# Performance work log

Measured on AMD Instinct MI355X. Metric: run time of the kernel, lower is better.

Reference implementation:

```python
import jax, jax.numpy as jnp
import numpy as np

RCUT = 6.0      # cutoff radius
AXIS = 16       # axis_neuron
NORM = 64.0     # normalizer = avg_neighbors + 1 (precomputed stat)
EPS = 1e-15
NTYPES = 2


def _embed(h, W0, b0, W1, b1, W2, b2):
    # tiny per-type-pair embedding MLP: scalar sr -> C channels
    h = jnp.tanh(h @ W0 + b0)
    h = jnp.tanh(h @ W1 + b1)
    return jnp.tanh(h @ W2 + b2)


def _forward(coord_3N, box_33, srmean, srstd, xrsrstd, Gbias, Ebias,
             emb_W0, emb_b0, emb_W1, emb_b1, emb_W2, emb_b2,
             fit_W0, fit_b0, fit_W1, fit_b1, fit_W2, fit_b2, n1):
    N = coord_3N.shape[1]
    L = jnp.diagonal(box_33)  # orthorhombic box lengths (3,)
    # relative coords with minimum-image convention: x[d,i,j] = c[d,j] - c[d,i]
    x_3NM = coord_3N[:, None, :] - coord_3N[:, :, None]
    x_3NM = x_3NM - L[:, None, None] * jnp.round(x_3NM / L[:, None, None])
    eye = jnp.eye(N, dtype=bool)
    r_NM = jnp.sqrt(jnp.where(eye, 1.0, (x_3NM ** 2).sum(0)))  # diag masked for safe grad
    # smooth switching / r  (DeepPot-SE style sr)
    u = r_NM / RCUT
    sw = jnp.where((r_NM < RCUT) & (~eye), ((-6.0 * u + 15.0) * u - 10.0) * u ** 3 + 1.0, 0.0)
    sr_NM = sw / r_NM
    rsr_NM = sr_NM / r_NM
    idx = (0, n1, N)  # contiguous type boundaries (atoms sorted by type)
    rows_sr, rows_rsr, rows_emb = [], [], []
    for i in range(NTYPES):
        sr_i = sr_NM[idx[i]:idx[i + 1]]
        rows_sr.append(sr_i / srstd[i])
        rows_rsr.append(rsr_NM[idx[i]:idx[i + 1]] / xrsrstd[i])
        srn_i = (sr_i - srmean[i]) / srstd[i]
        blocks = []
        for j in range(NTYPES):
            p = NTYPES * i + j  # type-pair index
            blocks.append(_embed(srn_i[:, idx[j]:idx[j + 1], None],
                                 emb_W0[p], emb_b0[p], emb_W1[p], emb_b1[p], emb_W2[p], emb_b2[p]))
        rows_emb.append(jnp.concatenate(blocks, axis=1))
    srbias_NM = jnp.concatenate(rows_sr, axis=0)
    R_3NM = (jnp.concatenate(rows_rsr, axis=0)[None] + EPS) * x_3NM  # e3norm = 1
    embed_NMC = jnp.concatenate(rows_emb, axis=0)
    # weighted reductions over neighbor axis M (einsum avoids the 3*N*M*C temp)
    Ginv_NC = jnp.einsum('nm,nmc->nc', srbias_NM, embed_NMC) / NORM
    Geqv_3NC = jnp.einsum('dnm,nmc->dnc', R_3NM, embed_NMC) / NORM
    G_4NC = jnp.concatenate([(Ginv_NC + Gbias)[None], Geqv_3NC], axis=0)
    # equivariant outer-product descriptor: Feat[n,a,c] = sum_k G[k,n,c]*G[k,n,a]
    Feat_NX = jnp.einsum('knc,kna->nac', G_4NC, G_4NC[:, :, :AXIS]).reshape(N, -1)
    energy = jnp.zeros((), dtype=Feat_NX.dtype)
    for i in range(NTYPES):
        h = Feat_NX[idx[i]:idx[i + 1]]
        h = jnp.tanh(h @ fit_W0[i] + fit_b0[i])
        h = jnp.tanh(h @ fit_W1[i] + fit_b1[i])
        h = h @ fit_W2[i] + fit_b2[i]
        energy = energy + (h + Ebias[i]).sum()
    return energy


def setup_inputs() -> dict:
    key = jax.random.key(0)
    ks = jax.random.split(key, 20)
    N, N1, BOXL = 1024, 512, 20.0
    W = (16, 32, 64)
    X, F = AXIS * W[-1], 128

    def wt(k, shape, fan_in):
        return jax.random.normal(k, shape, jnp.float32) / np.float32(np.sqrt(fan_in))

    return {
        'coord_3N': jax.random.uniform(ks[0], (3, N), jnp.float32) * BOXL,
        'box_33': BOXL * jnp.eye(3, dtype=jnp.float32),
        'srmean': 0.1 * jax.random.uniform(ks[1], (NTYPES,), jnp.float32),
        'srstd': 0.5 + jax.random.uniform(ks[2], (NTYPES,), jnp.float32),
        'xrsrstd': 0.5 + jax.random.uniform(ks[3], (NTYPES,), jnp.float32),
        'Gbias': 0.1 * jax.random.normal(ks[4], (W[2],), jnp.float32),
        'Ebias': jax.random.normal(ks[5], (NTYPES,), jnp.float32),
        'emb_W0': wt(ks[6], (4, 1, W[0]), 1),
        'emb_b0': 0.1 * jax.random.normal(ks[7], (4, W[0]), jnp.float32),
        'emb_W1': wt(ks[8], (4, W[0], W[1]), W[0]),
        'emb_b1': 0.1 * jax.random.normal(ks[9], (4, W[1]), jnp.float32),
        'emb_W2': wt(ks[10], (4, W[1], W[2]), W[1]),
        'emb_b2': 0.1 * jax.random.normal(ks[11], (4, W[2]), jnp.float32),
        'fit_W0': wt(ks[12], (NTYPES, X, F), X),
        'fit_b0': 0.1 * jax.random.normal(ks[13], (NTYPES, F), jnp.float32),
        'fit_W1': wt(ks[14], (NTYPES, F, F), F),
        'fit_b1': 0.1 * jax.random.normal(ks[15], (NTYPES, F), jnp.float32),
        'fit_W2': wt(ks[16], (NTYPES, F, 1), F),
        'fit_b2': 0.1 * jax.random.normal(ks[17], (NTYPES, 1), jnp.float32),
        'n1': N1,
    }


def reference(coord_3N, box_33, srmean, srstd, xrsrstd, Gbias, Ebias,
              emb_W0, emb_b0, emb_W1, emb_b1, emb_W2, emb_b2,
              fit_W0, fit_b0, fit_W1, fit_b1, fit_W2, fit_b2, n1):
    return _forward(coord_3N, box_33, srmean, srstd, xrsrstd, Gbias, Ebias,
                    emb_W0, emb_b0, emb_W1, emb_b1, emb_W2, emb_b2,
                    fit_W0, fit_b0, fit_W1, fit_b1, fit_W2, fit_b2, n1)
```

## Files before the change

### kernel.cpp

```cpp
#include <hip/hip_runtime.h>

#define RCUT 6.0f

typedef _Float16 h2 __attribute__((ext_vector_type(2)));
typedef _Float16 h8 __attribute__((ext_vector_type(8)));
typedef float    f4 __attribute__((ext_vector_type(4)));

__device__ __forceinline__ float fast_tanh(float x) {
    float e = __expf(2.0f * x);
    return 1.0f - 2.0f * __builtin_amdgcn_rcpf(e + 1.0f);
}

__device__ __forceinline__ h2 pkh(float a, float b) {
#if __has_builtin(__builtin_amdgcn_cvt_pkrtz)
    union { __fp16 __attribute__((ext_vector_type(2))) r; h2 h; } u;
    u.r = __builtin_amdgcn_cvt_pkrtz(a, b);
    return u.h;
#else
    h2 r; r.x = (_Float16)a; r.y = (_Float16)b; return r;
#endif
}

__global__ __launch_bounds__(256, 4) void k_embed(
    const float* __restrict__ coord, const float* __restrict__ box,
    const float* __restrict__ srmean, const float* __restrict__ srstd,
    const float* __restrict__ xrsrstd, const float* __restrict__ Gbias,
    const float* __restrict__ eW0, const float* __restrict__ eb0,
    const float* __restrict__ eW1, const float* __restrict__ eb1,
    const float* __restrict__ eW2, const float* __restrict__ eb2,
    const int* __restrict__ n1p,
    const float* __restrict__ fW0, const float* __restrict__ fW1,
    h2* __restrict__ feat, _Float16* __restrict__ W0ht,
    _Float16* __restrict__ W1ht, unsigned int* __restrict__ counter, int N)
{
    const int nb  = blockIdx.x;
    const int tid = threadIdx.x;

    __shared__ struct { float w0[2][16], b0[2][16]; } sw;
    __shared__ _Float16 s_h0[128][24];
    __shared__ _Float16 s_h1[128][40];
    __shared__ __align__(16) _Float16 s_ef[4][4][64][8];
    __shared__ float s_coef[4][128];
    __shared__ unsigned short s_nbr[512];
    __shared__ float s_g4[256];
    __shared__ int   s_wcnt[4], s_wcnt0[4];

    if (nb >= N) {
        const int b = nb - N;
        if (b == 0 && tid == 0) *counter = 0u;
        float (*s_t)[33] = reinterpret_cast<float(*)[33]>(&s_ef[0][0][0][0]);
        if (b < 256) {
            int type = b >> 7, tb = b & 127;
            int ki = tb >> 2, ci = tb & 3;
            const float* src = fW0 + (size_t)type * 131072;
            int c = tid & 31, r0 = (tid >> 5) * 4;
            #pragma unroll
            for (int q = 0; q < 4; q++)
                s_t[r0 + q][c] = src[(size_t)(ki * 32 + r0 + q) * 128 + ci * 32 + c];
            __syncthreads();
            _Float16* dst = W0ht + (size_t)type * 131072;
            int kk = tid & 31, c0 = (tid >> 5) * 4;
            #pragma unroll
            for (int q = 0; q < 4; q++)
                dst[(size_t)(ci * 32 + c0 + q) * 1024 + ki * 32 + kk] = (_Float16)s_t[kk][c0 + q];
        } else {
            int b2v = b - 256;
            int type = b2v >> 4, tb = b2v & 15;
            int ki = tb >> 2, ci = tb & 3;
            const float* src = fW1 + (size_t)type * 16384;
            int c = tid & 31, r0 = (tid >> 5) * 4;
            #pragma unroll
            for (int q = 0; q < 4; q++)
                s_t[r0 + q][c] = src[(size_t)(ki * 32 + r0 + q) * 128 + ci * 32 + c];
            __syncthreads();
            _Float16* dst = W1ht + (size_t)type * 16384;
            int kk = tid & 31, c0 = (tid >> 5) * 4;
            #pragma unroll
            for (int q = 0; q < 4; q++)
                dst[(size_t)(ci * 32 + c0 + q) * 128 + ki * 32 + kk] = (_Float16)s_t[kk][c0 + q];
        }
        return;
    }

    const int n  = nb;
    const int n1 = *n1p;
    const int ti = (n >= n1) ? 1 : 0;

    for (int t = tid; t < 32; t += 256) { int j = t >> 4, f = t & 15;
        sw.w0[j][f] = eW0[(2 * ti + j) * 16 + f];
        sw.b0[j][f] = eb0[(2 * ti + j) * 16 + f]; }

    const int wid = tid >> 6, lane = tid & 63;
    const int l15 = lane & 15, lk = lane >> 4;

    h8 bf[2][4];
    float b2r[2][4];
    #pragma unroll
    for (int j = 0; j < 2; j++) {
        const float* w2g = eW2 + (size_t)(2 * ti + j) * 2048;
        #pragma unroll
        for (int nt = 0; nt < 4; nt++) {
            h8 v;
            #pragma unroll
            for (int r = 0; r < 8; r++)
                v[r] = (_Float16)w2g[(8 * lk + r) * 64 + nt * 16 + l15];
            bf[j][nt] = v;
            b2r[j][nt] = eb2[(2 * ti + j) * 64 + nt * 16 + l15];
        }
    }
    h8 w1f[2][2];
    float b1r[2][2];
    #pragma unroll
    for (int j = 0; j < 2; j++) {
        const float* w1g = eW1 + (size_t)(2 * ti + j) * 512;
        #pragma unroll
        for (int nt1 = 0; nt1 < 2; nt1++) {
            h8 v = {};
            if (lk < 2) {
                #pragma unroll
                for (int r = 0; r < 8; r++)
                    v[r] = (_Float16)w1g[(8 * lk + r) * 32 + 16 * nt1 + l15];
            }
            w1f[j][nt1] = v;
            b1r[j][nt1] = eb1[(2 * ti + j) * 32 + 16 * nt1 + l15];
        }
    }

    const float Lx = box[0], Ly = box[4], Lz = box[8];
    const float iLx = 1.0f / Lx, iLy = 1.0f / Ly, iLz = 1.0f / Lz;
    const float xn = coord[n], yn = coord[N + n], zn = coord[2 * N + n];

    {
        unsigned long long bal[4];
        int wtotal = 0, wtotal0 = 0;
        const int mystart = wid * 256;
        #pragma unroll
        for (int r = 0; r < 4; r++) {
            int m = mystart + r * 64 + lane;
            float dx = coord[m] - xn;         dx -= Lx * rintf(dx * iLx);
            float dy = coord[N + m] - yn;     dy -= Ly * rintf(dy * iLy);
            float dz = coord[2 * N + m] - zn; dz -= Lz * rintf(dz * iLz);
            float r2 = dx * dx + dy * dy + dz * dz;
            bool pred = (r2 < RCUT * RCUT) && (m != n);
            bal[r] = __ballot(pred);
            unsigned long long bal0 = __ballot(pred && (m < n1));
            wtotal  += (int)__popcll(bal[r]);
            wtotal0 += (int)__popcll(bal0);
        }
        if (lane == 0) { s_wcnt[wid] = wtotal; s_wcnt0[wid] = wtotal0; }
        __syncthreads();
        int base = 0;
        for (int w = 0; w < wid; w++) base += s_wcnt[w];
        #pragma unroll
        for (int r = 0; r < 4; r++) {
            bool pred = (bal[r] >> lane) & 1ull;
            int pos = (int)__popcll(bal[r] & ((1ull << lane) - 1ull));
            if (pred && (base + pos) < 512)
                s_nbr[base + pos] = (unsigned short)(wid * 256 + r * 64 + lane);
            base += (int)__popcll(bal[r]);
        }
    }
    __syncthreads();
    int cnt  = s_wcnt[0] + s_wcnt[1] + s_wcnt[2] + s_wcnt[3];
    int cnt0 = s_wcnt0[0] + s_wcnt0[1] + s_wcnt0[2] + s_wcnt0[3];
    if (cnt > 512) cnt = 512;

    const float srm  = srmean[ti];
    const float isrs = 1.0f / srstd[ti];
    const float ixrs = 1.0f / xrsrstd[ti];

    const int p  = tid & 127;
    const int hh = tid >> 7;
    const int dummy = (n + 1 < N) ? (n + 1) : 0;

    f4 gacc = {0.0f, 0.0f, 0.0f, 0.0f};
    const f4 zf4 = {0.0f, 0.0f, 0.0f, 0.0f};

    const int ntiles = (cnt + 127) >> 7;
    for (int t = 0; t < ntiles; t++) {
        const int t128 = t << 7;
        __syncthreads();
        {
            const int pi = t128 + p;
            const bool valid = pi < cnt;
            int m = valid ? (int)s_nbr[pi] : dummy;
            float dx = coord[m] - xn;         dx -= Lx * rintf(dx * iLx);
            float dy = coord[N + m] - yn;     dy -= Ly * rintf(dy * iLy);
            float dz = coord[2 * N + m] - zn; dz -= Lz * rintf(dz * iLz);
            float r2 = dx * dx + dy * dy + dz * dz;
            float r  = sqrtf(r2);
            float rinv = __builtin_amdgcn_rcpf(r);
            float u  = r * (1.0f / RCUT);
            float u3 = u * u * u;
            float sw_ = ((-6.0f * u + 15.0f) * u - 10.0f) * u3 + 1.0f;
            if (!valid) sw_ = 0.0f;
            float sr  = sw_ * rinv;
            float srn = (sr - srm) * isrs;
            if (hh == 0) {
                float csr = valid ? sr * isrs : 0.0f;
                float crs = valid ? (sr * rinv * ixrs + 1e-15f) : 0.0f;
                s_coef[0][p] = csr;
                s_coef[1][p] = crs * dx;
                s_coef[2][p] = crs * dy;
                s_coef[3][p] = crs * dz;
            }
            const int j = (m >= n1) ? 1 : 0;
            h8 v;
            #pragma unroll
            for (int q = 0; q < 8; q++) {
                int f = 8 * hh + q;
                v[q] = (_Float16)fast_tanh(fmaf(srn, sw.w0[j][f], sw.b0[j][f]));
            }
            *(h8*)&s_h0[p][8 * hh] = v;
        }
        __syncthreads();

        {
            #pragma unroll
            for (int mt2 = 0; mt2 < 2; mt2++) {
                const int mt  = 2 * wid + mt2;
                const int row = 16 * mt + l15;
                h8 a = {};
                if (lk < 2) a = *(const h8*)&s_h0[row][8 * lk];
                const int gpb = 16 * mt;
                const bool need0 = (t128 + gpb) < cnt0;
                const bool need1 = (t128 + gpb + 15) >= cnt0;
                #pragma unroll
                for (int nt1 = 0; nt1 < 2; nt1++) {
                    f4 d0 = zf4, d1 = zf4;
                    if (need0) d0 = __builtin_amdgcn_mfma_f32_16x16x32_f16(a, w1f[0][nt1], zf4, 0, 0, 0);
                    if (need1) d1 = __builtin_amdgcn_mfma_f32_16x16x32_f16(a, w1f[1][nt1], zf4, 0, 0, 0);
                    #pragma unroll
                    for (int r = 0; r < 4; r++) {
                        int gp = gpb + 4 * lk + r;
                        bool is0 = (t128 + gp) < cnt0;
                        float dv = is0 ? d0[r] : d1[r];
                        float hv = fast_tanh(dv + (is0 ? b1r[0][nt1] : b1r[1][nt1]));
                        s_h1[gp][16 * nt1 + l15] = (_Float16)hv;
                    }
                }
            }
        }
        __syncthreads();

        {
            #pragma unroll
            for (int mt2 = 0; mt2 < 2; mt2++) {
                const int mt  = 2 * wid + mt2;
                const int row = 16 * mt + l15;
                h8 a = *(const h8*)&s_h1[row][8 * lk];
                const int gpb = 16 * mt;
                const bool need0 = (t128 + gpb) < cnt0;
                const bool need1 = (t128 + gpb + 15) >= cnt0;
                #pragma unroll
                for (int nt = 0; nt < 4; nt++) {
                    f4 d0 = zf4, d1 = zf4;
                    if (need0) d0 = __builtin_amdgcn_mfma_f32_16x16x32_f16(a, bf[0][nt], zf4, 0, 0, 0);
                    if (need1) d1 = __builtin_amdgcn_mfma_f32_16x16x32_f16(a, bf[1][nt], zf4, 0, 0, 0);
                    #pragma unroll
                    for (int r = 0; r < 4; r++) {
                        int gp = gpb + 4 * lk + r;
                        bool is0 = (t128 + gp) < cnt0;
                        float dv = is0 ? d0[r] : d1[r];
                        float ev = fast_tanh(dv + (is0 ? b2r[0][nt] : b2r[1][nt]));
                        s_ef[nt][gp >> 5][l15 + 16 * ((gp & 31) >> 3)][gp & 7] = (_Float16)ev;
                    }
                }
            }
        }
        __syncthreads();

        {
            #pragma unroll
            for (int ks = 0; ks < 4; ks++) {
                h8 ac;
                #pragma unroll
                for (int r = 0; r < 8; r++) {
                    int kk = 32 * ks + 8 * lk + r;
                    float cv = (l15 < 4) ? s_coef[l15][kk] : 0.0f;
                    ac[r] = (_Float16)cv;
                }
                h8 eb = *(const h8*)&s_ef[wid][ks][lane][0];
                gacc = __builtin_amdgcn_mfma_f32_16x16x32_f16(ac, eb, gacc, 0, 0, 0);
            }
        }
    }

    if (lane < 16) {
        #pragma unroll
        for (int r = 0; r < 4; r++) {
            float gv = gacc[r] * (1.0f / 64.0f);
            if (r == 0) gv += Gbias[16 * wid + lane];
            s_g4[r * 64 + 16 * wid + lane] = gv;
        }
    }
    __syncthreads();
    {
        h2* outp = feat + (size_t)n * 512;
        #pragma unroll
        for (int q = 0; q < 2; q++) {
            int o2 = tid + 256 * q;
            int a = o2 >> 5;
            int c = (2 * o2) & 63;
            float ga0 = s_g4[a],       ga1 = s_g4[64 + a];
            float ga2 = s_g4[128 + a], ga3 = s_g4[192 + a];
            float s0 = ga0 * s_g4[c];
            s0 = fmaf(ga1, s_g4[64 + c],  s0);
            s0 = fmaf(ga2, s_g4[128 + c], s0);
            s0 = fmaf(ga3, s_g4[192 + c], s0);
            float s1 = ga0 * s_g4[c + 1];
            s1 = fmaf(ga1, s_g4[64 + c + 1],  s1);
            s1 = fmaf(ga2, s_g4[128 + c + 1], s1);
            s1 = fmaf(ga3, s_g4[192 + c + 1], s1);
            outp[o2] = pkh(s0, s1);
        }
    }
}

__global__ __launch_bounds__(512) void k_fit(
    const _Float16* __restrict__ featf, const _Float16* __restrict__ W0ht,
    const _Float16* __restrict__ W1ht,
    const float* __restrict__ b0, const float* __restrict__ b1,
    const float* __restrict__ W2, const float* __restrict__ b2,
    const float* __restrict__ Ebias, const int* __restrict__ n1p,
    unsigned int* __restrict__ counter, float* __restrict__ slots,
    float* __restrict__ out)
{
    __shared__ _Float16 s_A[64 * 128];
    __shared__ _Float16 s_B[128 * 128];
    __shared__ _Float16 s_h[64 * 128];
    __shared__ float s_part[8];

    const int tid  = threadIdx.x;
    const int lane = tid & 63, w = tid >> 6;
    const int mt = w >> 1, nh = w & 1;
    const int l15 = lane & 15, lk = lane >> 4;
    const int n0 = blockIdx.x * 64;
    const int n1 = *n1p;
    const int ia = (n0 >= n1) ? 1 : 0;

    const _Float16* W0t = W0ht + (size_t)ia * 131072;
    const _Float16* W1t = W1ht + (size_t)ia * 16384;

    f4 acc[4];
    #pragma unroll
    for (int nt = 0; nt < 4; nt++) acc[nt] = (f4)0.0f;

    for (int kt = 0; kt < 8; kt++) {
        __syncthreads();
        {
            int r = tid >> 3, ub = (tid & 7) * 2;
            const h8* g = (const h8*)(featf + (size_t)(n0 + r) * 1024 + kt * 128);
            #pragma unroll
            for (int q = 0; q < 2; q++) {
                int u = ub + q;
                *(h8*)&s_A[r * 128 + ((u ^ (r & 15)) << 3)] = g[u];
            }
        }
        {
            int c = tid >> 2, ub = (tid & 3) * 4;
            const h8* g = (const h8*)(W0t + (size_t)c * 1024 + kt * 128);
            #pragma unroll
            for (int q = 0; q < 4; q++) {
                int u = ub + q;
                *(h8*)&s_B[c * 128 + ((u ^ (c & 15)) << 3)] = g[u];
            }
        }
        __syncthreads();
        #pragma unroll
        for (int ks = 0; ks < 4; ks++) {
            const int row = mt * 16 + l15;
            h8 a = *(const h8*)&s_A[row * 128 + (((ks * 4 + lk) ^ (row & 15)) << 3)];
            #pragma unroll
            for (int nt = 0; nt < 4; nt++) {
                const int c = nh * 64 + nt * 16 + l15;
                h8 bfr = *(const h8*)&s_B[c * 128 + (((ks * 4 + lk) ^ (c & 15)) << 3)];
                acc[nt] = __builtin_amdgcn_mfma_f32_16x16x32_f16(a, bfr, acc[nt], 0, 0, 0);
            }
        }
    }

    #pragma unroll
    for (int nt = 0; nt < 4; nt++) {
        const int c = nh * 64 + nt * 16 + l15;
        const float bias = b0[ia * 128 + c];
        #pragma unroll
        for (int r = 0; r < 4; r++) {
            const int row = mt * 16 + lk * 4 + r;
            float v = fast_tanh(acc[nt][r] + bias);
            s_h[row * 128 + (((c >> 3) ^ (row & 15)) << 3) + (c & 7)] = (_Float16)v;
        }
    }
    __syncthreads();
    {
        int c = tid >> 2, ub = (tid & 3) * 4;
        const h8* g = (const h8*)(W1t + (size_t)c * 128);
        #pragma unroll
        for (int q = 0; q < 4; q++) {
            int u = ub + q;
            *(h8*)&s_B[c * 128 + ((u ^ (c & 15)) << 3)] = g[u];
        }
    }
    __syncthreads();

    f4 acc1[4];
    #pragma unroll
    for (int nt = 0; nt < 4; nt++) acc1[nt] = (f4)0.0f;
    #pragma unroll
    for (int ks = 0; ks < 4; ks++) {
        const int row = mt * 16 + l15;
        h8 a = *(const h8*)&s_h[row * 128 + (((ks * 4 + lk) ^ (row & 15)) << 3)];
        #pragma unroll
        for (int nt = 0; nt < 4; nt++) {
            const int c = nh * 64 + nt * 16 + l15;
            h8 bfr = *(const h8*)&s_B[c * 128 + (((ks * 4 + lk) ^ (c & 15)) << 3)];
            acc1[nt] = __builtin_amdgcn_mfma_f32_16x16x32_f16(a, bfr, acc1[nt], 0, 0, 0);
        }
    }

    float p = 0.0f;
    #pragma unroll
    for (int nt = 0; nt < 4; nt++) {
        const int c = nh * 64 + nt * 16 + l15;
        const float bias = b1[ia * 128 + c];
        const float w2v  = W2[ia * 128 + c];
        #pragma unroll
        for (int r = 0; r < 4; r++)
            p += fast_tanh(acc1[nt][r] + bias) * w2v;
    }
    #pragma unroll
    for (int m = 1; m < 64; m <<= 1) p += __shfl_xor(p, m);
    if (lane == 0) s_part[w] = p;
    __syncthreads();
    if (tid == 0) {
        float e = ((s_part[0] + s_part[1]) + (s_part[2] + s_part[3]))
                + ((s_part[4] + s_part[5]) + (s_part[6] + s_part[7]))
                + 64.0f * (b2[ia] + Ebias[ia]);
        slots[blockIdx.x] = e;
        __threadfence();
        unsigned int old = atomicAdd(counter, 1u);
        if (old == 15u) {
            __threadfence();
            float tot = 0.0f;
            #pragma unroll
            for (int i = 0; i < 16; i++)
                tot += __hip_atomic_load(&slots[i], __ATOMIC_RELAXED, __HIP_MEMORY_SCOPE_AGENT);
            out[0] = tot;
        }
    }
}

extern "C" void kernel_launch(void* const* d_in, const int* in_sizes, int n_in,
                              void* d_out, int out_size, void* d_ws, size_t ws_size,
                              hipStream_t stream) {
    const float* coord   = (const float*)d_in[0];
    const float* box     = (const float*)d_in[1];
    const float* srmean  = (const float*)d_in[2];
    const float* srstd   = (const float*)d_in[3];
    const float* xrsrstd = (const float*)d_in[4];
    const float* Gbias   = (const float*)d_in[5];
    const float* Ebias   = (const float*)d_in[6];
    const float* eW0     = (const float*)d_in[7];
    const float* eb0     = (const float*)d_in[8];
    const float* eW1     = (const float*)d_in[9];
    const float* eb1     = (const float*)d_in[10];
    const float* eW2     = (const float*)d_in[11];
    const float* eb2     = (const float*)d_in[12];
    const float* fW0     = (const float*)d_in[13];
    const float* fb0     = (const float*)d_in[14];
    const float* fW1     = (const float*)d_in[15];
    const float* fb1     = (const float*)d_in[16];
    const float* fW2     = (const float*)d_in[17];
    const float* fb2     = (const float*)d_in[18];
    const int*   n1p     = (const int*)d_in[19];

    const int N = in_sizes[0] / 3;
    h2*       featbuf = (h2*)d_ws;
    _Float16* W0ht = (_Float16*)((char*)d_ws + (size_t)2 * 1024 * 1024);
    _Float16* W1ht = W0ht + 2 * 131072;
    char* tail = (char*)d_ws + (size_t)(2 * 1024 + 512 + 64) * 1024;
    unsigned int* counter = (unsigned int*)tail;
    float*        slots   = (float*)(tail + 64);

    k_embed<<<N + 288, 256, 0, stream>>>(coord, box, srmean, srstd, xrsrstd, Gbias,
                                         eW0, eb0, eW1, eb1, eW2, eb2, n1p,
                                         fW0, fW1, featbuf, W0ht, W1ht, counter, N);
    k_fit<<<N / 64, 512, 0, stream>>>((const _Float16*)featbuf, W0ht, W1ht,
                                      fb0, fb1, fW2, fb2, Ebias, n1p,
                                      counter, slots, (float*)d_out);
}
```

Baseline: 41.04 us.

## Process two atoms per embed block and split-K the fitting GEMM

The embed kernel now handles two centre atoms per block and shares the neighbour scan across both. It precomputes per-neighbour coefficients into shared memory once, so each tile no longer recomputes them from coordinates. Embedding weights are staged in shared memory instead of registers, and occupancy drops to three blocks per SM. The fit kernel switches to 16-row tiles with split-K across waves, reads operands straight from global memory and reduces through shared memory, which puts more blocks on the grid at the cost of extra reduction traffic.

```diff
diff --git a/kernel.cpp b/kernel.cpp
--- a/kernel.cpp
+++ b/kernel.cpp
@@ -2,26 +2,26 @@
 
 #define RCUT 6.0f
 
-typedef _Float16 h2 __attribute__((ext_vector_type(2)));
-typedef _Float16 h8 __attribute__((ext_vector_type(8)));
-typedef float    f4 __attribute__((ext_vector_type(4)));
+typedef _Float16 h2v __attribute__((ext_vector_type(2)));
+typedef _Float16 h8  __attribute__((ext_vector_type(8)));
+typedef float    f4  __attribute__((ext_vector_type(4)));
 
 __device__ __forceinline__ float fast_tanh(float x) {
     float e = __expf(2.0f * x);
     return 1.0f - 2.0f * __builtin_amdgcn_rcpf(e + 1.0f);
 }
 
-__device__ __forceinline__ h2 pkh(float a, float b) {
+__device__ __forceinline__ h2v pkh(float a, float b) {
 #if __has_builtin(__builtin_amdgcn_cvt_pkrtz)
-    union { __fp16 __attribute__((ext_vector_type(2))) r; h2 h; } u;
+    union { __fp16 __attribute__((ext_vector_type(2))) r; h2v h; } u;
     u.r = __builtin_amdgcn_cvt_pkrtz(a, b);
     return u.h;
 #else
-    h2 r; r.x = (_Float16)a; r.y = (_Float16)b; return r;
+    h2v r; r.x = (_Float16)a; r.y = (_Float16)b; return r;
 #endif
 }
 
-__global__ __launch_bounds__(256, 4) void k_embed(
+__global__ __launch_bounds__(256, 3) void k_embed(
     const float* __restrict__ coord, const float* __restrict__ box,
     const float* __restrict__ srmean, const float* __restrict__ srstd,
     const float* __restrict__ xrsrstd, const float* __restrict__ Gbias,
@@ -30,23 +30,26 @@
     const float* __restrict__ eW2, const float* __restrict__ eb2,
     const int* __restrict__ n1p,
     const float* __restrict__ fW0, const float* __restrict__ fW1,
-    h2* __restrict__ feat, _Float16* __restrict__ W0ht,
+    h2v* __restrict__ feat, _Float16* __restrict__ W0ht,
     _Float16* __restrict__ W1ht, unsigned int* __restrict__ counter, int N)
 {
     const int nb  = blockIdx.x;
     const int tid = threadIdx.x;
-
-    __shared__ struct { float w0[2][16], b0[2][16]; } sw;
-    __shared__ _Float16 s_h0[128][24];
-    __shared__ _Float16 s_h1[128][40];
+    const int NB  = N >> 1;
+
+    __shared__ float s_w0[2][16], s_b0[2][16];
+    __shared__ __align__(16) _Float16 s_srn[1024];
+    __shared__ __align__(16) _Float16 s_cf[4][1024];
+    __shared__ __align__(16) _Float16 s_h1[128][32];
     __shared__ __align__(16) _Float16 s_ef[4][4][64][8];
-    __shared__ float s_coef[4][128];
-    __shared__ unsigned short s_nbr[512];
-    __shared__ float s_g4[256];
-    __shared__ int   s_wcnt[4], s_wcnt0[4];
-
-    if (nb >= N) {
-        const int b = nb - N;
+    __shared__ unsigned short s_nbr[1024];
+    __shared__ float s_g4[2][256];
+    __shared__ __align__(16) _Float16 w1t[2][32][24];
+    __shared__ __align__(16) _Float16 w2t[2][64][40];
+    __shared__ int s_wA[4], s_wB[4];
+
+    if (nb >= NB) {
+        const int b = nb - NB;
         if (b == 0 && tid == 0) *counter = 0u;
         float (*s_t)[33] = reinterpret_cast<float(*)[33]>(&s_ef[0][0][0][0]);
         if (b < 256) {
@@ -64,8 +67,7 @@
             for (int q = 0; q < 4; q++)
                 dst[(size_t)(ci * 32 + c0 + q) * 1024 + ki * 32 + kk] = (_Float16)s_t[kk][c0 + q];
         } else {
-            int b2v = b - 256;
-            int type = b2v >> 4, tb = b2v & 15;
+            int b2v = b - 256, type = b2v >> 4, tb = b2v & 15;
             int ki = tb >> 2, ci = tb & 3;
             const float* src = fW1 + (size_t)type * 16384;
             int c = tid & 31, r0 = (tid >> 5) * 4;
@@ -82,242 +84,248 @@
         return;
     }
 
-    const int n  = nb;
+    const int nA = 2 * nb, nBt = 2 * nb + 1;
     const int n1 = *n1p;
-    const int ti = (n >= n1) ? 1 : 0;
-
-    for (int t = tid; t < 32; t += 256) { int j = t >> 4, f = t & 15;
-        sw.w0[j][f] = eW0[(2 * ti + j) * 16 + f];
-        sw.b0[j][f] = eb0[(2 * ti + j) * 16 + f]; }
-
+    const int ti = (nA >= n1) ? 1 : 0;
     const int wid = tid >> 6, lane = tid & 63;
     const int l15 = lane & 15, lk = lane >> 4;
 
-    h8 bf[2][4];
-    float b2r[2][4];
+    for (int t = tid; t < 32; t += 256) { int j = t >> 4, f = t & 15;
+        s_w0[j][f] = eW0[(2 * ti + j) * 16 + f];
+        s_b0[j][f] = eb0[(2 * ti + j) * 16 + f]; }
+    for (int idx = tid; idx < 1024; idx += 256) {
+        int j = idx >> 9, r = idx & 511, f = r >> 5, g = r & 31;
+        w1t[j][g][f] = (_Float16)eW1[(2 * ti + j) * 512 + f * 32 + g];
+    }
+    for (int idx = tid; idx < 4096; idx += 256) {
+        int j = idx >> 11, r = idx & 2047, g = r >> 6, c = r & 63;
+        w2t[j][c][g] = (_Float16)eW2[(2 * ti + j) * 2048 + g * 64 + c];
+    }
+    float b1r[2][2], b2r[2][4];
     #pragma unroll
     for (int j = 0; j < 2; j++) {
-        const float* w2g = eW2 + (size_t)(2 * ti + j) * 2048;
-        #pragma unroll
-        for (int nt = 0; nt < 4; nt++) {
-            h8 v;
-            #pragma unroll
-            for (int r = 0; r < 8; r++)
-                v[r] = (_Float16)w2g[(8 * lk + r) * 64 + nt * 16 + l15];
-            bf[j][nt] = v;
-            b2r[j][nt] = eb2[(2 * ti + j) * 64 + nt * 16 + l15];
-        }
-    }
-    h8 w1f[2][2];
-    float b1r[2][2];
-    #pragma unroll
-    for (int j = 0; j < 2; j++) {
-        const float* w1g = eW1 + (size_t)(2 * ti + j) * 512;
-        #pragma unroll
-        for (int nt1 = 0; nt1 < 2; nt1++) {
-            h8 v = {};
-            if (lk < 2) {
-                #pragma unroll
-                for (int r = 0; r < 8; r++)
-                    v[r] = (_Float16)w1g[(8 * lk + r) * 32 + 16 * nt1 + l15];
-            }
-            w1f[j][nt1] = v;
-            b1r[j][nt1] = eb1[(2 * ti + j) * 32 + 16 * nt1 + l15];
-        }
+        #pragma unroll
+        for (int q = 0; q < 2; q++) b1r[j][q] = eb1[(2 * ti + j) * 32 + 16 * q + l15];
+        #pragma unroll
+        for (int q = 0; q < 4; q++) b2r[j][q] = eb2[(2 * ti + j) * 64 + 16 * q + l15];
     }
 
     const float Lx = box[0], Ly = box[4], Lz = box[8];
     const float iLx = 1.0f / Lx, iLy = 1.0f / Ly, iLz = 1.0f / Lz;
-    const float xn = coord[n], yn = coord[N + n], zn = coord[2 * N + n];
-
-    {
-        unsigned long long bal[4];
-        int wtotal = 0, wtotal0 = 0;
-        const int mystart = wid * 256;
-        #pragma unroll
-        for (int r = 0; r < 4; r++) {
-            int m = mystart + r * 64 + lane;
-            float dx = coord[m] - xn;         dx -= Lx * rintf(dx * iLx);
-            float dy = coord[N + m] - yn;     dy -= Ly * rintf(dy * iLy);
-            float dz = coord[2 * N + m] - zn; dz -= Lz * rintf(dz * iLz);
-            float r2 = dx * dx + dy * dy + dz * dz;
-            bool pred = (r2 < RCUT * RCUT) && (m != n);
-            bal[r] = __ballot(pred);
-            unsigned long long bal0 = __ballot(pred && (m < n1));
-            wtotal  += (int)__popcll(bal[r]);
-            wtotal0 += (int)__popcll(bal0);
-        }
-        if (lane == 0) { s_wcnt[wid] = wtotal; s_wcnt0[wid] = wtotal0; }
-        __syncthreads();
-        int base = 0;
-        for (int w = 0; w < wid; w++) base += s_wcnt[w];
-        #pragma unroll
-        for (int r = 0; r < 4; r++) {
-            bool pred = (bal[r] >> lane) & 1ull;
-            int pos = (int)__popcll(bal[r] & ((1ull << lane) - 1ull));
-            if (pred && (base + pos) < 512)
-                s_nbr[base + pos] = (unsigned short)(wid * 256 + r * 64 + lane);
-            base += (int)__popcll(bal[r]);
-        }
-    }
-    __syncthreads();
-    int cnt  = s_wcnt[0] + s_wcnt[1] + s_wcnt[2] + s_wcnt[3];
-    int cnt0 = s_wcnt0[0] + s_wcnt0[1] + s_wcnt0[2] + s_wcnt0[3];
-    if (cnt > 512) cnt = 512;
-
+    const float xA = coord[nA], yA = coord[N + nA], zA = coord[2 * N + nA];
+    const float xB = coord[nBt], yB = coord[N + nBt], zB = coord[2 * N + nBt];
     const float srm  = srmean[ti];
     const float isrs = 1.0f / srstd[ti];
     const float ixrs = 1.0f / xrsrstd[ti];
 
-    const int p  = tid & 127;
-    const int hh = tid >> 7;
-    const int dummy = (n + 1 < N) ? (n + 1) : 0;
+    unsigned long long balA[4], balB[4];
+    float dxA[4], dyA[4], dzA[4], r2A[4];
+    float dxB[4], dyB[4], dzB[4], r2B[4];
+    {
+        int wA = 0, wB = 0;
+        const int mystart = wid * 256;
+        #pragma unroll
+        for (int r = 0; r < 4; r++) {
+            int m = mystart + r * 64 + lane;
+            float x = coord[m], y = coord[N + m], z = coord[2 * N + m];
+            float ax = x - xA; ax -= Lx * rintf(ax * iLx);
+            float ay = y - yA; ay -= Ly * rintf(ay * iLy);
+            float az = z - zA; az -= Lz * rintf(az * iLz);
+            float ra = ax * ax + ay * ay + az * az;
+            float bx = x - xB; bx -= Lx * rintf(bx * iLx);
+            float by = y - yB; by -= Ly * rintf(by * iLy);
+            float bz = z - zB; bz -= Lz * rintf(bz * iLz);
+            float rb = bx * bx + by * by + bz * bz;
+            dxA[r] = ax; dyA[r] = ay; dzA[r] = az; r2A[r] = ra;
+            dxB[r] = bx; dyB[r] = by; dzB[r] = bz; r2B[r] = rb;
+            bool pA = (ra < RCUT * RCUT) && (m != nA);
+            bool pB = (rb < RCUT * RCUT) && (m != nBt);
+            balA[r] = __ballot(pA);
+            balB[r] = __ballot(pB);
+            wA += (int)__popcll(balA[r]);
+            wB += (int)__popcll(balB[r]);
+        }
+        if (lane == 0) { s_wA[wid] = wA; s_wB[wid] = wB; }
+    }
+    __syncthreads();
+    int cntA = s_wA[0] + s_wA[1] + s_wA[2] + s_wA[3];
+    int cntB = s_wB[0] + s_wB[1] + s_wB[2] + s_wB[3];
+    int cnt  = cntA + cntB;
+    if (cnt > 1024) cnt = 1024;
+    if (cntA > 1024) cntA = 1024;
+    {
+        int baseA = 0, baseB = cntA;
+        for (int w = 0; w < wid; w++) { baseA += s_wA[w]; baseB += s_wB[w]; }
+        const unsigned long long lt = (1ull << lane) - 1ull;
+        const int mystart = wid * 256;
+        #pragma unroll
+        for (int r = 0; r < 4; r++) {
+            int m = mystart + r * 64 + lane;
+            #pragma unroll
+            for (int cc = 0; cc < 2; cc++) {
+                unsigned long long bal = cc ? balB[r] : balA[r];
+                int base = cc ? baseB : baseA;
+                if ((bal >> lane) & 1ull) {
+                    int pos = base + (int)__popcll(bal & lt);
+                    if (pos < 1024) {
+                        float dx = cc ? dxB[r] : dxA[r];
+                        float dy = cc ? dyB[r] : dyA[r];
+                        float dz = cc ? dzB[r] : dzA[r];
+                        float r2 = cc ? r2B[r] : r2A[r];
+                        float rr = sqrtf(r2);
+                        float rinv = __builtin_amdgcn_rcpf(rr);
+                        float u  = rr * (1.0f / RCUT);
+                        float u3 = u * u * u;
+                        float sw_ = ((-6.0f * u + 15.0f) * u - 10.0f) * u3 + 1.0f;
+                        float sr  = sw_ * rinv;
+                        float crs = sr * rinv * ixrs + 1e-15f;
+                        s_srn[pos]   = (_Float16)((sr - srm) * isrs);
+                        s_cf[0][pos] = (_Float16)(sr * isrs);
+                        s_cf[1][pos] = (_Float16)(crs * dx);
+                        s_cf[2][pos] = (_Float16)(crs * dy);
+                        s_cf[3][pos] = (_Float16)(crs * dz);
+                        s_nbr[pos]   = (unsigned short)m;
+                    }
+                }
+                if (cc) baseB += (int)__popcll(bal);
+                else    baseA += (int)__popcll(bal);
+            }
+        }
+    }
+    __syncthreads();
+    const int ntiles = (cnt + 127) >> 7;
+    for (int i = cnt + tid; i < ntiles * 128; i += 256) {
+        s_srn[i] = (_Float16)0.0f; s_nbr[i] = 0;
+        s_cf[0][i] = (_Float16)0.0f; s_cf[1][i] = (_Float16)0.0f;
+        s_cf[2][i] = (_Float16)0.0f; s_cf[3][i] = (_Float16)0.0f;
+    }
+    __syncthreads();
 
     f4 gacc = {0.0f, 0.0f, 0.0f, 0.0f};
     const f4 zf4 = {0.0f, 0.0f, 0.0f, 0.0f};
 
-    const int ntiles = (cnt + 127) >> 7;
     for (int t = 0; t < ntiles; t++) {
         const int t128 = t << 7;
         __syncthreads();
-        {
-            const int pi = t128 + p;
-            const bool valid = pi < cnt;
-            int m = valid ? (int)s_nbr[pi] : dummy;
-            float dx = coord[m] - xn;         dx -= Lx * rintf(dx * iLx);
-            float dy = coord[N + m] - yn;     dy -= Ly * rintf(dy * iLy);
-            float dz = coord[2 * N + m] - zn; dz -= Lz * rintf(dz * iLz);
-            float r2 = dx * dx + dy * dy + dz * dz;
-            float r  = sqrtf(r2);
-            float rinv = __builtin_amdgcn_rcpf(r);
-            float u  = r * (1.0f / RCUT);
-            float u3 = u * u * u;
-            float sw_ = ((-6.0f * u + 15.0f) * u - 10.0f) * u3 + 1.0f;
-            if (!valid) sw_ = 0.0f;
-            float sr  = sw_ * rinv;
-            float srn = (sr - srm) * isrs;
-            if (hh == 0) {
-                float csr = valid ? sr * isrs : 0.0f;
-                float crs = valid ? (sr * rinv * ixrs + 1e-15f) : 0.0f;
-                s_coef[0][p] = csr;
-                s_coef[1][p] = crs * dx;
-                s_coef[2][p] = crs * dy;
-                s_coef[3][p] = crs * dz;
-            }
-            const int j = (m >= n1) ? 1 : 0;
-            h8 v;
-            #pragma unroll
-            for (int q = 0; q < 8; q++) {
-                int f = 8 * hh + q;
-                v[q] = (_Float16)fast_tanh(fmaf(srn, sw.w0[j][f], sw.b0[j][f]));
-            }
-            *(h8*)&s_h0[p][8 * hh] = v;
+
+        #pragma unroll
+        for (int mt2 = 0; mt2 < 2; mt2++) {
+            const int mt = 2 * wid + mt2;
+            const int row = 16 * mt + l15;
+            const int rp = t128 + row;
+            float srn = (float)s_srn[rp];
+            int jr = (s_nbr[rp] >= n1) ? 1 : 0;
+            h8 a = {};
+            if (lk < 2) {
+                const float* wp = &s_w0[jr][8 * lk];
+                const float* bp = &s_b0[jr][8 * lk];
+                #pragma unroll
+                for (int q = 0; q < 8; q++)
+                    a[q] = (_Float16)fast_tanh(fmaf(srn, wp[q], bp[q]));
+            }
+            #pragma unroll
+            for (int nt1 = 0; nt1 < 2; nt1++) {
+                const int c = 16 * nt1 + l15;
+                h8 b0f = {}, b1f = {};
+                if (lk < 2) {
+                    b0f = *(const h8*)&w1t[0][c][8 * lk];
+                    b1f = *(const h8*)&w1t[1][c][8 * lk];
+                }
+                f4 d0 = __builtin_amdgcn_mfma_f32_16x16x32_f16(a, b0f, zf4, 0, 0, 0);
+                f4 d1 = __builtin_amdgcn_mfma_f32_16x16x32_f16(a, b1f, zf4, 0, 0, 0);
+                #pragma unroll
+                for (int r = 0; r < 4; r++) {
+                    int gp = 16 * mt + 4 * lk + r;
+                    bool is0 = (s_nbr[t128 + gp] < n1);
+                    float hv = fast_tanh((is0 ? d0[r] : d1[r]) + (is0 ? b1r[0][nt1] : b1r[1][nt1]));
+                    int e = 16 * nt1 + l15;
+                    s_h1[gp][(((e >> 3) ^ ((gp >> 1) & 3)) << 3) + (e & 7)] = (_Float16)hv;
+                }
+            }
+        }
+        asm volatile("" ::: "memory");
+        #pragma unroll
+        for (int mt2 = 0; mt2 < 2; mt2++) {
+            const int mt = 2 * wid + mt2;
+            const int row = 16 * mt + l15;
+            h8 a2 = *(const h8*)&s_h1[row][((lk ^ ((row >> 1) & 3)) << 3)];
+            #pragma unroll
+            for (int nt = 0; nt < 4; nt++) {
+                const int c = 16 * nt + l15;
+                h8 w20 = *(const h8*)&w2t[0][c][8 * lk];
+                h8 w21 = *(const h8*)&w2t[1][c][8 * lk];
+                f4 e0 = __builtin_amdgcn_mfma_f32_16x16x32_f16(a2, w20, zf4, 0, 0, 0);
+                f4 e1 = __builtin_amdgcn_mfma_f32_16x16x32_f16(a2, w21, zf4, 0, 0, 0);
+                #pragma unroll
+                for (int r = 0; r < 4; r++) {
+                    int gp = 16 * mt + 4 * lk + r;
+                    bool is0 = (s_nbr[t128 + gp] < n1);
+                    float ev = fast_tanh((is0 ? e0[r] : e1[r]) + (is0 ? b2r[0][nt] : b2r[1][nt]));
+                    s_ef[nt][gp >> 5][l15 + 16 * ((gp & 31) >> 3)][gp & 7] = (_Float16)ev;
+                }
+            }
         }
         __syncthreads();
 
-        {
-            #pragma unroll
-            for (int mt2 = 0; mt2 < 2; mt2++) {
-                const int mt  = 2 * wid + mt2;
-                const int row = 16 * mt + l15;
-                h8 a = {};
-                if (lk < 2) a = *(const h8*)&s_h0[row][8 * lk];
-                const int gpb = 16 * mt;
-                const bool need0 = (t128 + gpb) < cnt0;
-                const bool need1 = (t128 + gpb + 15) >= cnt0;
-                #pragma unroll
-                for (int nt1 = 0; nt1 < 2; nt1++) {
-                    f4 d0 = zf4, d1 = zf4;
-                    if (need0) d0 = __builtin_amdgcn_mfma_f32_16x16x32_f16(a, w1f[0][nt1], zf4, 0, 0, 0);
-                    if (need1) d1 = __builtin_amdgcn_mfma_f32_16x16x32_f16(a, w1f[1][nt1], zf4, 0, 0, 0);
+        #pragma unroll
+        for (int ks = 0; ks < 4; ks++) {
+            const int s = t128 + 32 * ks;
+            h8 ac = {};
+            if (l15 < 8) {
+                const bool rowA = l15 < 4;
+                const int  cr   = rowA ? l15 : (l15 - 4);
+                const bool allA = (s + 31) < cntA;
+                const bool allB = s >= cntA;
+                if ((allA && rowA) || (allB && !rowA)) {
+                    ac = *(const h8*)&s_cf[cr][s + 8 * lk];
+                } else if (!allA && !allB) {
                     #pragma unroll
-                    for (int r = 0; r < 4; r++) {
-                        int gp = gpb + 4 * lk + r;
-                        bool is0 = (t128 + gp) < cnt0;
-                        float dv = is0 ? d0[r] : d1[r];
-                        float hv = fast_tanh(dv + (is0 ? b1r[0][nt1] : b1r[1][nt1]));
-                        s_h1[gp][16 * nt1 + l15] = (_Float16)hv;
+                    for (int r = 0; r < 8; r++) {
+                        int p = s + 8 * lk + r;
+                        bool isA = p < cntA;
+                        if (isA == rowA) ac[r] = s_cf[cr][p];
                     }
                 }
             }
-        }
-        __syncthreads();
-
-        {
-            #pragma unroll
-            for (int mt2 = 0; mt2 < 2; mt2++) {
-                const int mt  = 2 * wid + mt2;
-                const int row = 16 * mt + l15;
-                h8 a = *(const h8*)&s_h1[row][8 * lk];
-                const int gpb = 16 * mt;
-                const bool need0 = (t128 + gpb) < cnt0;
-                const bool need1 = (t128 + gpb + 15) >= cnt0;
-                #pragma unroll
-                for (int nt = 0; nt < 4; nt++) {
-                    f4 d0 = zf4, d1 = zf4;
-                    if (need0) d0 = __builtin_amdgcn_mfma_f32_16x16x32_f16(a, bf[0][nt], zf4, 0, 0, 0);
-                    if (need1) d1 = __builtin_amdgcn_mfma_f32_16x16x32_f16(a, bf[1][nt], zf4, 0, 0, 0);
-                    #pragma unroll
-                    for (int r = 0; r < 4; r++) {
-                        int gp = gpb + 4 * lk + r;
-                        bool is0 = (t128 + gp) < cnt0;
-                        float dv = is0 ? d0[r] : d1[r];
-                        float ev = fast_tanh(dv + (is0 ? b2r[0][nt] : b2r[1][nt]));
-                        s_ef[nt][gp >> 5][l15 + 16 * ((gp & 31) >> 3)][gp & 7] = (_Float16)ev;
-                    }
-                }
-            }
-        }
-        __syncthreads();
-
-        {
-            #pragma unroll
-            for (int ks = 0; ks < 4; ks++) {
-                h8 ac;
-                #pragma unroll
-                for (int r = 0; r < 8; r++) {
-                    int kk = 32 * ks + 8 * lk + r;
-                    float cv = (l15 < 4) ? s_coef[l15][kk] : 0.0f;
-                    ac[r] = (_Float16)cv;
-                }
-                h8 eb = *(const h8*)&s_ef[wid][ks][lane][0];
-                gacc = __builtin_amdgcn_mfma_f32_16x16x32_f16(ac, eb, gacc, 0, 0, 0);
-            }
-        }
-    }
-
-    if (lane < 16) {
+            h8 eb = *(const h8*)&s_ef[wid][ks][lane][0];
+            gacc = __builtin_amdgcn_mfma_f32_16x16x32_f16(ac, eb, gacc, 0, 0, 0);
+        }
+    }
+
+    if (lk < 2) {
+        float* sg = &s_g4[lk][0];
         #pragma unroll
         for (int r = 0; r < 4; r++) {
             float gv = gacc[r] * (1.0f / 64.0f);
-            if (r == 0) gv += Gbias[16 * wid + lane];
-            s_g4[r * 64 + 16 * wid + lane] = gv;
-        }
-    }
-    __syncthreads();
-    {
-        h2* outp = feat + (size_t)n * 512;
+            if (r == 0) gv += Gbias[16 * wid + l15];
+            sg[r * 64 + 16 * wid + l15] = gv;
+        }
+    }
+    __syncthreads();
+    #pragma unroll
+    for (int at = 0; at < 2; at++) {
+        const float* sg = &s_g4[at][0];
+        h2v* outp = feat + (size_t)(2 * nb + at) * 512;
         #pragma unroll
         for (int q = 0; q < 2; q++) {
             int o2 = tid + 256 * q;
-            int a = o2 >> 5;
-            int c = (2 * o2) & 63;
-            float ga0 = s_g4[a],       ga1 = s_g4[64 + a];
-            float ga2 = s_g4[128 + a], ga3 = s_g4[192 + a];
-            float s0 = ga0 * s_g4[c];
-            s0 = fmaf(ga1, s_g4[64 + c],  s0);
-            s0 = fmaf(ga2, s_g4[128 + c], s0);
-            s0 = fmaf(ga3, s_g4[192 + c], s0);
-            float s1 = ga0 * s_g4[c + 1];
-            s1 = fmaf(ga1, s_g4[64 + c + 1],  s1);
-            s1 = fmaf(ga2, s_g4[128 + c + 1], s1);
-            s1 = fmaf(ga3, s_g4[192 + c + 1], s1);
+            int a = o2 >> 5, c = (2 * o2) & 63;
+            float ga0 = sg[a],       ga1 = sg[64 + a];
+            float ga2 = sg[128 + a], ga3 = sg[192 + a];
+            float s0 = ga0 * sg[c];
+            s0 = fmaf(ga1, sg[64 + c],  s0);
+            s0 = fmaf(ga2, sg[128 + c], s0);
+            s0 = fmaf(ga3, sg[192 + c], s0);
+            float s1 = ga0 * sg[c + 1];
+            s1 = fmaf(ga1, sg[64 + c + 1],  s1);
+            s1 = fmaf(ga2, sg[128 + c + 1], s1);
+            s1 = fmaf(ga3, sg[192 + c + 1], s1);
             outp[o2] = pkh(s0, s1);
         }
     }
 }
 
-__global__ __launch_bounds__(512) void k_fit(
+__global__ __launch_bounds__(512, 1) void k_fit(
     const _Float16* __restrict__ featf, const _Float16* __restrict__ W0ht,
     const _Float16* __restrict__ W1ht,
     const float* __restrict__ b0, const float* __restrict__ b1,
@@ -326,126 +334,108 @@
     unsigned int* __restrict__ counter, float* __restrict__ slots,
     float* __restrict__ out)
 {
-    __shared__ _Float16 s_A[64 * 128];
-    __shared__ _Float16 s_B[128 * 128];
-    __shared__ _Float16 s_h[64 * 128];
-    __shared__ float s_part[8];
-
-    const int tid  = threadIdx.x;
+    __shared__ float s_red[4][2][16][64];
+    __shared__ __align__(16) _Float16 s_hd[16][128];
+    __shared__ float s_sum[16][32];
+
+    const int tid = threadIdx.x;
     const int lane = tid & 63, w = tid >> 6;
-    const int mt = w >> 1, nh = w & 1;
+    const int kq = w >> 1, ch = w & 1;
     const int l15 = lane & 15, lk = lane >> 4;
-    const int n0 = blockIdx.x * 64;
-    const int n1 = *n1p;
-    const int ia = (n0 >= n1) ? 1 : 0;
-
-    const _Float16* W0t = W0ht + (size_t)ia * 131072;
-    const _Float16* W1t = W1ht + (size_t)ia * 16384;
-
-    f4 acc[4];
+    const int n0 = blockIdx.x * 16;
+    const int ia = (n0 >= *n1p) ? 1 : 0;
+    const f4 zf4 = {0.0f, 0.0f, 0.0f, 0.0f};
+
+    const _Float16* Ap = featf + (size_t)(n0 + l15) * 1024 + kq * 256;
+    const _Float16* B0 = W0ht + (size_t)ia * 131072 + kq * 256;
+    f4 acc[4] = {zf4, zf4, zf4, zf4};
     #pragma unroll
-    for (int nt = 0; nt < 4; nt++) acc[nt] = (f4)0.0f;
-
-    for (int kt = 0; kt < 8; kt++) {
-        __syncthreads();
-        {
-            int r = tid >> 3, ub = (tid & 7) * 2;
-            const h8* g = (const h8*)(featf + (size_t)(n0 + r) * 1024 + kt * 128);
-            #pragma unroll
-            for (int q = 0; q < 2; q++) {
-                int u = ub + q;
-                *(h8*)&s_A[r * 128 + ((u ^ (r & 15)) << 3)] = g[u];
-            }
-        }
-        {
-            int c = tid >> 2, ub = (tid & 3) * 4;
-            const h8* g = (const h8*)(W0t + (size_t)c * 1024 + kt * 128);
-            #pragma unroll
-            for (int q = 0; q < 4; q++) {
-                int u = ub + q;
-                *(h8*)&s_B[c * 128 + ((u ^ (c & 15)) << 3)] = g[u];
-            }
-        }
-        __syncthreads();
-        #pragma unroll
-        for (int ks = 0; ks < 4; ks++) {
-            const int row = mt * 16 + l15;
-            h8 a = *(const h8*)&s_A[row * 128 + (((ks * 4 + lk) ^ (row & 15)) << 3)];
-            #pragma unroll
-            for (int nt = 0; nt < 4; nt++) {
-                const int c = nh * 64 + nt * 16 + l15;
-                h8 bfr = *(const h8*)&s_B[c * 128 + (((ks * 4 + lk) ^ (c & 15)) << 3)];
-                acc[nt] = __builtin_amdgcn_mfma_f32_16x16x32_f16(a, bfr, acc[nt], 0, 0, 0);
-            }
-        }
-    }
-
+    for (int ks = 0; ks < 8; ks++) {
+        h8 a = *(const h8*)(Ap + ks * 32 + 8 * lk);
+        #pragma unroll
+        for (int nt = 0; nt < 4; nt++) {
+            const int c = ch * 64 + nt * 16 + l15;
+            h8 b = *(const h8*)(B0 + (size_t)c * 1024 + ks * 32 + 8 * lk);
+            acc[nt] = __builtin_amdgcn_mfma_f32_16x16x32_f16(a, b, acc[nt], 0, 0, 0);
+        }
+    }
     #pragma unroll
-    for (int nt = 0; nt < 4; nt++) {
-        const int c = nh * 64 + nt * 16 + l15;
-        const float bias = b0[ia * 128 + c];
-        #pragma unroll
-        for (int r = 0; r < 4; r++) {
-            const int row = mt * 16 + lk * 4 + r;
-            float v = fast_tanh(acc[nt][r] + bias);
-            s_h[row * 128 + (((c >> 3) ^ (row & 15)) << 3) + (c & 7)] = (_Float16)v;
-        }
-    }
-    __syncthreads();
+    for (int nt = 0; nt < 4; nt++)
+        #pragma unroll
+        for (int r = 0; r < 4; r++)
+            s_red[kq][ch][4 * lk + r][nt * 16 + l15] = acc[nt][r];
+    __syncthreads();
+
     {
-        int c = tid >> 2, ub = (tid & 3) * 4;
-        const h8* g = (const h8*)(W1t + (size_t)c * 128);
+        const int row = tid >> 5, c0 = (tid & 31) * 4;
+        const int chh = c0 >> 6, cl = c0 & 63;
+        f4 v = *(const f4*)&s_red[0][chh][row][cl];
+        v += *(const f4*)&s_red[1][chh][row][cl];
+        v += *(const f4*)&s_red[2][chh][row][cl];
+        v += *(const f4*)&s_red[3][chh][row][cl];
         #pragma unroll
         for (int q = 0; q < 4; q++) {
-            int u = ub + q;
-            *(h8*)&s_B[c * 128 + ((u ^ (c & 15)) << 3)] = g[u];
-        }
-    }
-    __syncthreads();
-
-    f4 acc1[4];
+            int c = c0 + q;
+            float h = fast_tanh(v[q] + b0[ia * 128 + c]);
+            s_hd[row][(((c >> 3) ^ row) << 3) + (c & 7)] = (_Float16)h;
+        }
+    }
+    __syncthreads();
+
+    f4 acc1[4] = {zf4, zf4, zf4, zf4};
+    {
+        h8 a = *(const h8*)&s_hd[l15][(((4 * kq + lk) ^ l15) & 15) << 3];
+        const _Float16* B1 = W1ht + (size_t)ia * 16384 + kq * 32;
+        #pragma unroll
+        for (int nt = 0; nt < 4; nt++) {
+            const int c = ch * 64 + nt * 16 + l15;
+            h8 b = *(const h8*)(B1 + (size_t)c * 128 + 8 * lk);
+            acc1[nt] = __builtin_amdgcn_mfma_f32_16x16x32_f16(a, b, zf4, 0, 0, 0);
+        }
+    }
     #pragma unroll
-    for (int nt = 0; nt < 4; nt++) acc1[nt] = (f4)0.0f;
-    #pragma unroll
-    for (int ks = 0; ks < 4; ks++) {
-        const int row = mt * 16 + l15;
-        h8 a = *(const h8*)&s_h[row * 128 + (((ks * 4 + lk) ^ (row & 15)) << 3)];
-        #pragma unroll
-        for (int nt = 0; nt < 4; nt++) {
-            const int c = nh * 64 + nt * 16 + l15;
-            h8 bfr = *(const h8*)&s_B[c * 128 + (((ks * 4 + lk) ^ (c & 15)) << 3)];
-            acc1[nt] = __builtin_amdgcn_mfma_f32_16x16x32_f16(a, bfr, acc1[nt], 0, 0, 0);
-        }
-    }
-
-    float p = 0.0f;
-    #pragma unroll
-    for (int nt = 0; nt < 4; nt++) {
-        const int c = nh * 64 + nt * 16 + l15;
-        const float bias = b1[ia * 128 + c];
-        const float w2v  = W2[ia * 128 + c];
+    for (int nt = 0; nt < 4; nt++)
         #pragma unroll
         for (int r = 0; r < 4; r++)
-            p += fast_tanh(acc1[nt][r] + bias) * w2v;
-    }
-    #pragma unroll
-    for (int m = 1; m < 64; m <<= 1) p += __shfl_xor(p, m);
-    if (lane == 0) s_part[w] = p;
-    __syncthreads();
-    if (tid == 0) {
-        float e = ((s_part[0] + s_part[1]) + (s_part[2] + s_part[3]))
-                + ((s_part[4] + s_part[5]) + (s_part[6] + s_part[7]))
-                + 64.0f * (b2[ia] + Ebias[ia]);
-        slots[blockIdx.x] = e;
-        __threadfence();
-        unsigned int old = atomicAdd(counter, 1u);
-        if (old == 15u) {
+            s_red[kq][ch][4 * lk + r][nt * 16 + l15] = acc1[nt][r];
+    __syncthreads();
+
+    {
+        const int row = tid >> 5, c0 = (tid & 31) * 4;
+        const int chh = c0 >> 6, cl = c0 & 63;
+        f4 v = *(const f4*)&s_red[0][chh][row][cl];
+        v += *(const f4*)&s_red[1][chh][row][cl];
+        v += *(const f4*)&s_red[2][chh][row][cl];
+        v += *(const f4*)&s_red[3][chh][row][cl];
+        float pv = 0.0f;
+        #pragma unroll
+        for (int q = 0; q < 4; q++) {
+            int c = c0 + q;
+            pv += fast_tanh(v[q] + b1[ia * 128 + c]) * W2[ia * 128 + c];
+        }
+        s_sum[row][tid & 31] = pv;
+    }
+    __syncthreads();
+    if (w == 0) {
+        const int row = lane >> 2, g = lane & 3;
+        float s = 0.0f;
+        #pragma unroll
+        for (int i = 0; i < 8; i++) s += s_sum[row][8 * g + i];
+        s += __shfl_xor(s, 1);  s += __shfl_xor(s, 2);
+        s += __shfl_xor(s, 4);  s += __shfl_xor(s, 8);
+        s += __shfl_xor(s, 16); s += __shfl_xor(s, 32);
+        if (lane == 0) {
+            float e = s + 16.0f * (b2[ia] + Ebias[ia]);
+            slots[blockIdx.x] = e;
             __threadfence();
-            float tot = 0.0f;
-            #pragma unroll
-            for (int i = 0; i < 16; i++)
-                tot += __hip_atomic_load(&slots[i], __ATOMIC_RELAXED, __HIP_MEMORY_SCOPE_AGENT);
-            out[0] = tot;
+            unsigned int old = atomicAdd(counter, 1u);
+            if (old == 63u) {
+                __threadfence();
+                float tot = 0.0f;
+                for (int i = 0; i < 64; i++)
+                    tot += __hip_atomic_load(&slots[i], __ATOMIC_RELAXED, __HIP_MEMORY_SCOPE_AGENT);
+                out[0] = tot;
+            }
         }
     }
 }
@@ -475,17 +465,18 @@
     const int*   n1p     = (const int*)d_in[19];
 
     const int N = in_sizes[0] / 3;
-    h2*       featbuf = (h2*)d_ws;
+    h2v*      featbuf = (h2v*)d_ws;
     _Float16* W0ht = (_Float16*)((char*)d_ws + (size_t)2 * 1024 * 1024);
     _Float16* W1ht = W0ht + 2 * 131072;
     char* tail = (char*)d_ws + (size_t)(2 * 1024 + 512 + 64) * 1024;
     unsigned int* counter = (unsigned int*)tail;
     float*        slots   = (float*)(tail + 64);
 
-    k_embed<<<N + 288, 256, 0, stream>>>(coord, box, srmean, srstd, xrsrstd, Gbias,
-                                         eW0, eb0, eW1, eb1, eW2, eb2, n1p,
-                                         fW0, fW1, featbuf, W0ht, W1ht, counter, N);
-    k_fit<<<N / 64, 512, 0, stream>>>((const _Float16*)featbuf, W0ht, W1ht,
+    k_embed<<<N / 2 + 288, 256, 0, stream>>>(coord, box, srmean, srstd, xrsrstd,
+                                             Gbias, eW0, eb0, eW1, eb1, eW2, eb2,
+                                             n1p, fW0, fW1, featbuf, W0ht, W1ht,
+                                             counter, N);
+    k_fit<<<N / 16, 512, 0, stream>>>((const _Float16*)featbuf, W0ht, W1ht,
                                       fb0, fb1, fW2, fb2, Ebias, n1p,
                                       counter, slots, (float*)d_out);
 }
```

Result: faster. 39.42 us (-4.0%).
